# Kernel optimization log

Hardware: AMD Instinct MI355X
Metric: run time of the kernel (lower is better)

## Reference

```python
import jax, jax.numpy as jnp
import numpy as np

NB_KNN = (10, 20, 100, 200)   # values of k to evaluate; max_k = 200
T = 0.07                       # softmax temperature
NUM_CLASSES = 1000


def setup_inputs() -> dict:
    key = jax.random.key(0)
    k1, k2, k3 = jax.random.split(key, 3)
    features_rank = jax.random.normal(k1, (256, 512), jnp.float32)      # (B, d) query features
    train_features = jax.random.normal(k2, (100000, 512), jnp.float32)  # (N, d) train bank
    train_labels = jax.random.randint(k3, (100000,), 0, NUM_CLASSES)     # (N,) int labels
    return {"features_rank": features_rank, "train_features": train_features,
            "train_labels": train_labels}


def _knn_probs(features_rank, train_features, train_labels):
    max_k = max(NB_KNN)
    # similarity: (B, N) = (B, d) @ (d, N)  -- mirrors torch.mm(broadcasted, train_features_rank_T)
    sims = features_rank @ train_features.T
    topk_sims, idx = jax.lax.top_k(sims, max_k)          # (B, max_k), sorted descending
    neighbors = train_labels[idx]                         # (B, max_k) gathered labels
    w = jax.nn.softmax(topk_sims / T, axis=1)             # (B, max_k) neighbor weights
    B = features_rank.shape[0]
    rows = jnp.arange(B)[:, None]                         # (B, 1) row indices for scatter
    # Instead of materializing one_hot (B, max_k, C) and summing prefixes,
    # scatter-add the first k weights into per-class buckets (same math, fused).
    probs = [jnp.zeros((B, NUM_CLASSES), w.dtype).at[rows, neighbors[:, :k]].add(w[:, :k])
             for k in NB_KNN]
    return jnp.stack(probs, axis=0)                       # (len(NB_KNN), B, C)


def reference(features_rank, train_features, train_labels):
    return _knn_probs(features_rank, train_features, train_labels)
```

## Files before the change

kernel.cpp:

```cpp
#include <hip/hip_runtime.h>
#include <math.h>

#define KDIM   512
#define NCLS   1000
#define CUTOFF 3.0f
#define MAXCAP 4096
#define BN     64
#define BK     64
#define NSTAGE (KDIM / BK)
#define FCAP   512

typedef __attribute__((ext_vector_type(8))) short  short8;
typedef __attribute__((ext_vector_type(4))) float  floatx4;

__device__ __forceinline__ unsigned enc_f(float f) {
    unsigned u = __float_as_uint(f);
    return (u & 0x80000000u) ? ~u : (u | 0x80000000u);
}
__device__ __forceinline__ float dec_f(unsigned k) {
    unsigned u = (k & 0x80000000u) ? (k & 0x7FFFFFFFu) : ~k;
    return __uint_as_float(u);
}
__device__ __forceinline__ unsigned short f2bf(float f) {
    unsigned u = __float_as_uint(f);
    u += 0x7FFFu + ((u >> 16) & 1u);
    return (unsigned short)(u >> 16);
}
__device__ __forceinline__ float bf2f(unsigned short h) {
    return __uint_as_float(((unsigned)h) << 16);
}

__global__ void k_prep(const float* __restrict__ A, unsigned short* __restrict__ af,
                       unsigned* __restrict__ cnt, unsigned* __restrict__ gmax, int Brows) {
    int t = blockIdx.x * blockDim.x + threadIdx.x;
    if (t < Brows) { cnt[t] = 0u; gmax[t] = enc_f(-3.0e38f); }
    if (t >= Brows * (KDIM / 8)) return;
    int r = t >> 6;
    int o = t & 63;
    int s16 = r >> 4, c = o >> 2, kq = o & 3;
    int lane = kq * 16 + (r & 15);
    const float* src = A + (size_t)r * KDIM + o * 8;
    size_t bhi = ((size_t)((s16 * 16 + c) * 2 + 0) * 64 + lane) * 8;
    size_t blo = ((size_t)((s16 * 16 + c) * 2 + 1) * 64 + lane) * 8;
#pragma unroll
    for (int j = 0; j < 8; ++j) {
        float f = src[j];
        unsigned short h = f2bf(f);
        af[bhi + j] = h;
        af[blo + j] = f2bf(f - bf2f(h));
    }
}

__global__ __launch_bounds__(256, 3) void k_gemm(
    const float* __restrict__ Bt,
    const unsigned short* __restrict__ af,
    float* __restrict__ cand_val, int* __restrict__ cand_idx,
    unsigned* __restrict__ cnt, unsigned* __restrict__ gmax,
    int N, int cap)
{
    __shared__ short8 BsH[2][512];
    __shared__ short8 BsL[2][512];

    const int tid  = threadIdx.x;
    const int lane = tid & 63;
    const int wid  = tid >> 6;
    const int colBase = blockIdx.x * BN;

    const int nl   = tid >> 2;
    const int kseg = (tid & 3) * 16;
    const int gcol = colBase + nl;
    const bool colok = (gcol < N);
    const float* bsrc = Bt + (size_t)gcol * KDIM + kseg;

    int slotw[2];
#pragma unroll
    for (int oo = 0; oo < 2; ++oo) {
        const int k8  = kseg + oo * 8;
        const int chw = k8 >> 5;
        const int kqw = (k8 >> 3) & 3;
        const int ctw = (nl >> 4) & 3;
        const int fidw = chw * 4 + ctw;
        const int lfw  = kqw * 16 + (nl & 15);
        slotw[oo] = fidw * 64 + (lfw ^ (kqw * 2 + chw));
    }

    floatx4 acc[4][4];
#pragma unroll
    for (int rt = 0; rt < 4; ++rt)
#pragma unroll
        for (int ct = 0; ct < 4; ++ct)
            acc[rt][ct] = (floatx4){0.f, 0.f, 0.f, 0.f};

    const float4 z4 = make_float4(0.f, 0.f, 0.f, 0.f);
    float4 c0 = colok ? *(const float4*)(bsrc)           : z4;
    float4 c1 = colok ? *(const float4*)(bsrc + 4)       : z4;
    float4 c2 = colok ? *(const float4*)(bsrc + 8)       : z4;
    float4 c3 = colok ? *(const float4*)(bsrc + 12)      : z4;
    float4 n0 = colok ? *(const float4*)(bsrc + BK)      : z4;
    float4 n1 = colok ? *(const float4*)(bsrc + BK + 4)  : z4;
    float4 n2 = colok ? *(const float4*)(bsrc + BK + 8)  : z4;
    float4 n3 = colok ? *(const float4*)(bsrc + BK + 12) : z4;

    auto cvw = [&](int buf, float4 a0, float4 a1, float4 a2, float4 a3) {
        union { float4 v[4]; float f[16]; } P;
        P.v[0] = a0; P.v[1] = a1; P.v[2] = a2; P.v[3] = a3;
#pragma unroll
        for (int oo = 0; oo < 2; ++oo) {
            union { short8 v; unsigned short u[8]; } H, L;
#pragma unroll
            for (int j = 0; j < 8; ++j) {
                float f = P.f[oo * 8 + j];
                unsigned short h = f2bf(f);
                H.u[j] = h; L.u[j] = f2bf(f - bf2f(h));
            }
            BsH[buf][slotw[oo]] = H.v;
            BsL[buf][slotw[oo]] = L.v;
        }
    };

    cvw(0, c0, c1, c2, c3);
    __syncthreads();

    for (int s = 0; s < NSTAGE; ++s) {
        if (s + 1 < NSTAGE) {
            c0 = n0; c1 = n1; c2 = n2; c3 = n3;
            if (s + 2 < NSTAGE) {
                const float* p = bsrc + (s + 2) * BK;
                n0 = colok ? *(const float4*)(p)      : z4;
                n1 = colok ? *(const float4*)(p + 4)  : z4;
                n2 = colok ? *(const float4*)(p + 8)  : z4;
                n3 = colok ? *(const float4*)(p + 12) : z4;
            }
            cvw((s + 1) & 1, c0, c1, c2, c3);
        }

#pragma unroll
        for (int chunk = 0; chunk < 2; ++chunk) {
            const int cg = s * 2 + chunk;
            short8 aH[4], aL[4];
#pragma unroll
            for (int rt = 0; rt < 4; ++rt) {
                const int s16 = wid * 4 + rt;
                size_t sl = (size_t)((s16 * 16 + cg) * 2) * 64 + lane;
                aH[rt] = *(const short8*)(af + sl * 8);
                aL[rt] = *(const short8*)(af + (sl + 64) * 8);
            }
            const int g = (lane >> 4) * 2 + chunk;
#pragma unroll
            for (int ct = 0; ct < 4; ++ct) {
                const int idx = (chunk * 4 + ct) * 64 + (lane ^ g);
                short8 bh = BsH[s & 1][idx];
                short8 bl = BsL[s & 1][idx];
#pragma unroll
                for (int rt = 0; rt < 4; ++rt) {
                    acc[rt][ct] = __builtin_amdgcn_mfma_f32_16x16x32_bf16(aH[rt], bh, acc[rt][ct], 0, 0, 0);
                    acc[rt][ct] = __builtin_amdgcn_mfma_f32_16x16x32_bf16(aH[rt], bl, acc[rt][ct], 0, 0, 0);
                    acc[rt][ct] = __builtin_amdgcn_mfma_f32_16x16x32_bf16(aL[rt], bh, acc[rt][ct], 0, 0, 0);
                }
            }
        }
        __syncthreads();
    }

    const int q   = lane >> 4;
    const int n15 = lane & 15;
#pragma unroll
    for (int rt = 0; rt < 4; ++rt) {
#pragma unroll
        for (int reg = 0; reg < 4; ++reg) {
            const int row = wid * 64 + rt * 16 + q * 4 + reg;
            float m = fmaxf(fmaxf(acc[rt][0][reg], acc[rt][1][reg]),
                            fmaxf(acc[rt][2][reg], acc[rt][3][reg]));
#pragma unroll
            for (int off = 1; off < 16; off <<= 1) m = fmaxf(m, __shfl_xor(m, off));
            unsigned oldk = 0u;
            if (n15 == 0) oldk = atomicMax(&gmax[row], enc_f(m));
            oldk = (unsigned)__shfl((int)oldk, lane & 48);
            const float thr = fmaxf(dec_f(oldk), m) - CUTOFF;
#pragma unroll
            for (int ct = 0; ct < 4; ++ct) {
                const float v = acc[rt][ct][reg];
                const int col = colBase + ct * 16 + n15;
                if (v >= thr && col < N) {
                    unsigned p = atomicAdd(&cnt[row], 1u);
                    if (p < (unsigned)cap) {
                        cand_val[(size_t)row * cap + p] = v;
                        cand_idx[(size_t)row * cap + p] = col;
                    }
                }
            }
        }
    }
}

__global__ __launch_bounds__(256) void k_finalize(
    const float* __restrict__ cand_val,
    const int* __restrict__ cand_idx,
    const unsigned* __restrict__ cnt,
    const unsigned* __restrict__ gmax,
    const int* __restrict__ labels,
    float* __restrict__ out,
    int Brows, int cap)
{
    __shared__ float s_val[FCAP];
    __shared__ int   s_idx[FCAP];
    __shared__ float s_out[4 * NCLS];
    __shared__ int   s_n;
    __shared__ float s_part[4];
    __shared__ float s_Z;

    const int row = blockIdx.x;
    const int tid = threadIdx.x;
    if (tid == 0) s_n = 0;
    __syncthreads();

    const float m   = dec_f(gmax[row]);
    const float thr = m - CUTOFF;
    const int n = min((int)cnt[row], cap);
    for (int i = tid; i < n; i += 256) {
        float v = cand_val[(size_t)row * cap + i];
        if (v >= thr) {
            int p = atomicAdd(&s_n, 1);
            if (p < FCAP) { s_val[p] = v; s_idx[p] = cand_idx[(size_t)row * cap + i]; }
        }
    }
    for (int c = tid; c < 4 * NCLS; c += 256) s_out[c] = 0.f;
    __syncthreads();
    const int ns = min(s_n, FCAP);

    float e0 = 0.f, e1 = 0.f;
    int   r0 = 0x7fffffff, r1 = 0x7fffffff;
    int   lab0 = 0, lab1 = 0;
    if (tid < ns) {
        const float v = s_val[tid]; const int ix = s_idx[tid];
        int rk = 0;
        for (int j = 0; j < ns; ++j) {
            const float vj = s_val[j];
            rk += (vj > v || (vj == v && s_idx[j] < ix)) ? 1 : 0;
        }
        r0 = rk;
        if (rk < 200) { e0 = expf((v - m) * (1.0f / 0.07f)); lab0 = labels[ix]; }
    }
    if (tid + 256 < ns) {
        const int i2 = tid + 256;
        const float v = s_val[i2]; const int ix = s_idx[i2];
        int rk = 0;
        for (int j = 0; j < ns; ++j) {
            const float vj = s_val[j];
            rk += (vj > v || (vj == v && s_idx[j] < ix)) ? 1 : 0;
        }
        r1 = rk;
        if (rk < 200) { e1 = expf((v - m) * (1.0f / 0.07f)); lab1 = labels[ix]; }
    }

    float part = e0 + e1;
#pragma unroll
    for (int off = 32; off >= 1; off >>= 1) part += __shfl_down(part, off);
    if ((tid & 63) == 0) s_part[tid >> 6] = part;
    __syncthreads();
    if (tid == 0) s_Z = (s_part[0] + s_part[1]) + (s_part[2] + s_part[3]);
    __syncthreads();
    const float invZ = 1.0f / s_Z;

    if (r0 < 200) {
        const float w = e0 * invZ;
        if (r0 < 10)  atomicAdd(&s_out[0 * NCLS + lab0], w);
        if (r0 < 20)  atomicAdd(&s_out[1 * NCLS + lab0], w);
        if (r0 < 100) atomicAdd(&s_out[2 * NCLS + lab0], w);
        atomicAdd(&s_out[3 * NCLS + lab0], w);
    }
    if (r1 < 200) {
        const float w = e1 * invZ;
        if (r1 < 10)  atomicAdd(&s_out[0 * NCLS + lab1], w);
        if (r1 < 20)  atomicAdd(&s_out[1 * NCLS + lab1], w);
        if (r1 < 100) atomicAdd(&s_out[2 * NCLS + lab1], w);
        atomicAdd(&s_out[3 * NCLS + lab1], w);
    }
    __syncthreads();

    for (int c = tid; c < 4 * NCLS; c += 256) {
        const int sl = c / NCLS, cc = c - sl * NCLS;
        out[(size_t)sl * ((size_t)Brows * NCLS) + (size_t)row * NCLS + cc] = s_out[c];
    }
}

extern "C" void kernel_launch(void* const* d_in, const int* in_sizes, int n_in,
                              void* d_out, int out_size, void* d_ws, size_t ws_size,
                              hipStream_t stream) {
    const float* A      = (const float*)d_in[0];
    const float* Bt     = (const float*)d_in[1];
    const int*   labels = (const int*)d_in[2];
    float* out = (float*)d_out;

    const int Brows = in_sizes[0] / KDIM;
    const int N     = in_sizes[2];

    size_t af_elems = (size_t)Brows * KDIM * 2;
    unsigned short* af = (unsigned short*)d_ws;
    unsigned* cnt  = (unsigned*)(af + af_elems);
    unsigned* gmax = cnt + Brows;
    char* rest = (char*)(gmax + Brows);
    size_t used  = (size_t)(rest - (char*)d_ws);
    size_t avail = (ws_size > used) ? (ws_size - used) : 0;
    int cap = (int)((avail / ((size_t)Brows * 8)) < (size_t)MAXCAP
                        ? (avail / ((size_t)Brows * 8)) : (size_t)MAXCAP);
    if (cap < 1) cap = 1;
    float* cand_val = (float*)rest;
    int*   cand_idx = (int*)(cand_val + (size_t)Brows * cap);

    k_prep<<<(Brows * (KDIM / 8) + 255) / 256, 256, 0, stream>>>(A, af, cnt, gmax, Brows);
    k_gemm<<<(N + BN - 1) / BN, 256, 0, stream>>>(Bt, af, cand_val, cand_idx, cnt, gmax, N, cap);
    k_finalize<<<Brows, 256, 0, stream>>>(cand_val, cand_idx, cnt, gmax, labels, out, Brows, cap);
}
```

Measured before the change: 412.2 us.

## Widen GEMM column tile to 128 with 8 waves each covering 32 rows

The similarity GEMM block now handles 128 train columns with 512 threads (8 waves) instead of 64 columns with 256 threads. Each wave covers 32 query rows by 128 columns (2x8 MFMA tiles) rather than 64x64. This halves the number of blocks, so each block re-reads the bf16-split A operand from global memory for twice as many columns, and the per-wave A fragment loads are cut in half. The cost is double the LDS per block and a different register mix, which may change occupancy, and each wave now reads more B fragments from LDS.

Result: faster. 385.5 us (-6.5%).

```diff
diff --git a/kernel.cpp b/kernel.cpp
--- a/kernel.cpp
+++ b/kernel.cpp
@@ -5,7 +5,7 @@
 #define NCLS   1000
 #define CUTOFF 3.0f
 #define MAXCAP 4096
-#define BN     64
+#define BN     128
 #define BK     64
 #define NSTAGE (KDIM / BK)
 #define FCAP   512
@@ -51,108 +51,103 @@
     }
 }
 
-__global__ __launch_bounds__(256, 3) void k_gemm(
+__global__ __launch_bounds__(512, 3) void k_gemm(
     const float* __restrict__ Bt,
     const unsigned short* __restrict__ af,
     float* __restrict__ cand_val, int* __restrict__ cand_idx,
     unsigned* __restrict__ cnt, unsigned* __restrict__ gmax,
     int N, int cap)
 {
-    __shared__ short8 BsH[2][512];
-    __shared__ short8 BsL[2][512];
+    __shared__ short8 BsH[2][1024];
+    __shared__ short8 BsL[2][1024];
 
     const int tid  = threadIdx.x;
     const int lane = tid & 63;
     const int wid  = tid >> 6;
     const int colBase = blockIdx.x * BN;
 
-    const int nl   = tid >> 2;
-    const int kseg = (tid & 3) * 16;
-    const int gcol = colBase + nl;
-    const bool colok = (gcol < N);
-    const float* bsrc = Bt + (size_t)gcol * KDIM + kseg;
-
-    int slotw[2];
-#pragma unroll
-    for (int oo = 0; oo < 2; ++oo) {
-        const int k8  = kseg + oo * 8;
-        const int chw = k8 >> 5;
-        const int kqw = (k8 >> 3) & 3;
-        const int ctw = (nl >> 4) & 3;
-        const int fidw = chw * 4 + ctw;
-        const int lfw  = kqw * 16 + (nl & 15);
-        slotw[oo] = fidw * 64 + (lfw ^ (kqw * 2 + chw));
-    }
-
-    floatx4 acc[4][4];
-#pragma unroll
-    for (int rt = 0; rt < 4; ++rt)
-#pragma unroll
-        for (int ct = 0; ct < 4; ++ct)
+    const int nl  = tid >> 3;
+    const int k8  = (tid & 7) * 8;
+    const int gcol0 = colBase + nl;
+    const int gcol1 = colBase + 64 + nl;
+    const bool ok0 = (gcol0 < N);
+    const bool ok1 = (gcol1 < N);
+    const float* bsrc0 = Bt + (size_t)gcol0 * KDIM + k8;
+    const float* bsrc1 = Bt + (size_t)gcol1 * KDIM + k8;
+    const int chw = k8 >> 5;
+    const int kqw = (k8 >> 3) & 3;
+    const int ctw = (nl >> 4) & 3;
+    const int fidw = chw * 4 + ctw;
+    const int lfw  = kqw * 16 + (nl & 15);
+    const int slotw = fidw * 64 + (lfw ^ (kqw * 2 + chw));
+
+    floatx4 acc[2][8];
+#pragma unroll
+    for (int rt = 0; rt < 2; ++rt)
+#pragma unroll
+        for (int ct = 0; ct < 8; ++ct)
             acc[rt][ct] = (floatx4){0.f, 0.f, 0.f, 0.f};
 
     const float4 z4 = make_float4(0.f, 0.f, 0.f, 0.f);
-    float4 c0 = colok ? *(const float4*)(bsrc)           : z4;
-    float4 c1 = colok ? *(const float4*)(bsrc + 4)       : z4;
-    float4 c2 = colok ? *(const float4*)(bsrc + 8)       : z4;
-    float4 c3 = colok ? *(const float4*)(bsrc + 12)      : z4;
-    float4 n0 = colok ? *(const float4*)(bsrc + BK)      : z4;
-    float4 n1 = colok ? *(const float4*)(bsrc + BK + 4)  : z4;
-    float4 n2 = colok ? *(const float4*)(bsrc + BK + 8)  : z4;
-    float4 n3 = colok ? *(const float4*)(bsrc + BK + 12) : z4;
-
-    auto cvw = [&](int buf, float4 a0, float4 a1, float4 a2, float4 a3) {
-        union { float4 v[4]; float f[16]; } P;
-        P.v[0] = a0; P.v[1] = a1; P.v[2] = a2; P.v[3] = a3;
-#pragma unroll
-        for (int oo = 0; oo < 2; ++oo) {
-            union { short8 v; unsigned short u[8]; } H, L;
-#pragma unroll
-            for (int j = 0; j < 8; ++j) {
-                float f = P.f[oo * 8 + j];
-                unsigned short h = f2bf(f);
-                H.u[j] = h; L.u[j] = f2bf(f - bf2f(h));
-            }
-            BsH[buf][slotw[oo]] = H.v;
-            BsL[buf][slotw[oo]] = L.v;
-        }
+    float4 c00 = ok0 ? *(const float4*)(bsrc0)          : z4;
+    float4 c01 = ok0 ? *(const float4*)(bsrc0 + 4)      : z4;
+    float4 c10 = ok1 ? *(const float4*)(bsrc1)          : z4;
+    float4 c11 = ok1 ? *(const float4*)(bsrc1 + 4)      : z4;
+    float4 n00 = ok0 ? *(const float4*)(bsrc0 + BK)     : z4;
+    float4 n01 = ok0 ? *(const float4*)(bsrc0 + BK + 4) : z4;
+    float4 n10 = ok1 ? *(const float4*)(bsrc1 + BK)     : z4;
+    float4 n11 = ok1 ? *(const float4*)(bsrc1 + BK + 4) : z4;
+
+    auto cvw = [&](int buf, int off, float4 a0, float4 a1) {
+        union { float4 v[2]; float f[8]; } P;
+        union { short8 v; unsigned short u[8]; } H, L;
+        P.v[0] = a0; P.v[1] = a1;
+#pragma unroll
+        for (int j = 0; j < 8; ++j) {
+            unsigned short h = f2bf(P.f[j]);
+            H.u[j] = h; L.u[j] = f2bf(P.f[j] - bf2f(h));
+        }
+        BsH[buf][off + slotw] = H.v; BsL[buf][off + slotw] = L.v;
     };
 
-    cvw(0, c0, c1, c2, c3);
+    cvw(0, 0,   c00, c01);
+    cvw(0, 512, c10, c11);
     __syncthreads();
 
     for (int s = 0; s < NSTAGE; ++s) {
         if (s + 1 < NSTAGE) {
-            c0 = n0; c1 = n1; c2 = n2; c3 = n3;
+            c00 = n00; c01 = n01; c10 = n10; c11 = n11;
             if (s + 2 < NSTAGE) {
-                const float* p = bsrc + (s + 2) * BK;
-                n0 = colok ? *(const float4*)(p)      : z4;
-                n1 = colok ? *(const float4*)(p + 4)  : z4;
-                n2 = colok ? *(const float4*)(p + 8)  : z4;
-                n3 = colok ? *(const float4*)(p + 12) : z4;
+                const float* p0 = bsrc0 + (s + 2) * BK;
+                const float* p1 = bsrc1 + (s + 2) * BK;
+                n00 = ok0 ? *(const float4*)(p0)     : z4;
+                n01 = ok0 ? *(const float4*)(p0 + 4) : z4;
+                n10 = ok1 ? *(const float4*)(p1)     : z4;
+                n11 = ok1 ? *(const float4*)(p1 + 4) : z4;
             }
-            cvw((s + 1) & 1, c0, c1, c2, c3);
+            cvw((s + 1) & 1, 0,   c00, c01);
+            cvw((s + 1) & 1, 512, c10, c11);
         }
 
 #pragma unroll
         for (int chunk = 0; chunk < 2; ++chunk) {
             const int cg = s * 2 + chunk;
-            short8 aH[4], aL[4];
-#pragma unroll
-            for (int rt = 0; rt < 4; ++rt) {
-                const int s16 = wid * 4 + rt;
+            short8 aH[2], aL[2];
+#pragma unroll
+            for (int rt = 0; rt < 2; ++rt) {
+                const int s16 = wid * 2 + rt;
                 size_t sl = (size_t)((s16 * 16 + cg) * 2) * 64 + lane;
                 aH[rt] = *(const short8*)(af + sl * 8);
                 aL[rt] = *(const short8*)(af + (sl + 64) * 8);
             }
             const int g = (lane >> 4) * 2 + chunk;
 #pragma unroll
-            for (int ct = 0; ct < 4; ++ct) {
-                const int idx = (chunk * 4 + ct) * 64 + (lane ^ g);
+            for (int ct = 0; ct < 8; ++ct) {
+                const int idx = (chunk * 4 + (ct & 3)) * 64 + (lane ^ g) + ((ct & 4) ? 512 : 0);
                 short8 bh = BsH[s & 1][idx];
                 short8 bl = BsL[s & 1][idx];
 #pragma unroll
-                for (int rt = 0; rt < 4; ++rt) {
+                for (int rt = 0; rt < 2; ++rt) {
                     acc[rt][ct] = __builtin_amdgcn_mfma_f32_16x16x32_bf16(aH[rt], bh, acc[rt][ct], 0, 0, 0);
                     acc[rt][ct] = __builtin_amdgcn_mfma_f32_16x16x32_bf16(aH[rt], bl, acc[rt][ct], 0, 0, 0);
                     acc[rt][ct] = __builtin_amdgcn_mfma_f32_16x16x32_bf16(aL[rt], bh, acc[rt][ct], 0, 0, 0);
@@ -165,12 +160,13 @@
     const int q   = lane >> 4;
     const int n15 = lane & 15;
 #pragma unroll
-    for (int rt = 0; rt < 4; ++rt) {
+    for (int rt = 0; rt < 2; ++rt) {
 #pragma unroll
         for (int reg = 0; reg < 4; ++reg) {
-            const int row = wid * 64 + rt * 16 + q * 4 + reg;
-            float m = fmaxf(fmaxf(acc[rt][0][reg], acc[rt][1][reg]),
-                            fmaxf(acc[rt][2][reg], acc[rt][3][reg]));
+            const int row = wid * 32 + rt * 16 + q * 4 + reg;
+            float m = acc[rt][0][reg];
+#pragma unroll
+            for (int ct = 1; ct < 8; ++ct) m = fmaxf(m, acc[rt][ct][reg]);
 #pragma unroll
             for (int off = 1; off < 16; off <<= 1) m = fmaxf(m, __shfl_xor(m, off));
             unsigned oldk = 0u;
@@ -178,9 +174,9 @@
             oldk = (unsigned)__shfl((int)oldk, lane & 48);
             const float thr = fmaxf(dec_f(oldk), m) - CUTOFF;
 #pragma unroll
-            for (int ct = 0; ct < 4; ++ct) {
+            for (int ct = 0; ct < 8; ++ct) {
                 const float v = acc[rt][ct][reg];
-                const int col = colBase + ct * 16 + n15;
+                const int col = colBase + ((ct & 4) ? 64 : 0) + (ct & 3) * 16 + n15;
                 if (v >= thr && col < N) {
                     unsigned p = atomicAdd(&cnt[row], 1u);
                     if (p < (unsigned)cap) {
@@ -309,6 +305,6 @@
     int*   cand_idx = (int*)(cand_val + (size_t)Brows * cap);
 
     k_prep<<<(Brows * (KDIM / 8) + 255) / 256, 256, 0, stream>>>(A, af, cnt, gmax, Brows);
-    k_gemm<<<(N + BN - 1) / BN, 256, 0, stream>>>(Bt, af, cand_val, cand_idx, cnt, gmax, N, cap);
+    k_gemm<<<(N + BN - 1) / BN, 512, 0, stream>>>(Bt, af, cand_val, cand_idx, cnt, gmax, N, cap);
     k_finalize<<<Brows, 256, 0, stream>>>(cand_val, cand_idx, cnt, gmax, labels, out, Brows, cap);
 }
```

## Use 512-thread GEMM blocks with halved per-wave row tiles and hoisted A loads

Applied to the files above, without the earlier changes.

Doubles the GEMM block to 8 waves, so each wave covers 32 query rows instead of 64 and each thread converts 8 B elements per stage instead of 16. The A fragments for both chunks are now loaded before the B conversion and the block barrier, and MFMA issue priority is raised during the inner loop. The aim is lower register pressure and more waves in flight to hide global and LDS latency. Each block still covers the same columns, so there are more waves contending for the same LDS tile and one extra barrier per stage.

Result: faster. 386.2 us (-6.3%).

```diff
diff --git a/kernel.cpp b/kernel.cpp
--- a/kernel.cpp
+++ b/kernel.cpp
@@ -51,7 +51,7 @@
     }
 }
 
-__global__ __launch_bounds__(256, 3) void k_gemm(
+__global__ __launch_bounds__(512, 4) void k_gemm(
     const float* __restrict__ Bt,
     const unsigned short* __restrict__ af,
     float* __restrict__ cand_val, int* __restrict__ cand_idx,
@@ -66,85 +66,81 @@
     const int wid  = tid >> 6;
     const int colBase = blockIdx.x * BN;
 
-    const int nl   = tid >> 2;
-    const int kseg = (tid & 3) * 16;
+    const int nl  = tid >> 3;
+    const int k8  = (tid & 7) * 8;
     const int gcol = colBase + nl;
     const bool colok = (gcol < N);
-    const float* bsrc = Bt + (size_t)gcol * KDIM + kseg;
-
-    int slotw[2];
-#pragma unroll
-    for (int oo = 0; oo < 2; ++oo) {
-        const int k8  = kseg + oo * 8;
-        const int chw = k8 >> 5;
-        const int kqw = (k8 >> 3) & 3;
-        const int ctw = (nl >> 4) & 3;
-        const int fidw = chw * 4 + ctw;
-        const int lfw  = kqw * 16 + (nl & 15);
-        slotw[oo] = fidw * 64 + (lfw ^ (kqw * 2 + chw));
-    }
-
-    floatx4 acc[4][4];
-#pragma unroll
-    for (int rt = 0; rt < 4; ++rt)
+    const float* bsrc = Bt + (size_t)gcol * KDIM + k8;
+    const int chw = k8 >> 5;
+    const int kqw = (k8 >> 3) & 3;
+    const int ctw = (nl >> 4) & 3;
+    const int fidw = chw * 4 + ctw;
+    const int lfw  = kqw * 16 + (nl & 15);
+    const int slotw = fidw * 64 + (lfw ^ (kqw * 2 + chw));
+
+    floatx4 acc[2][4];
+#pragma unroll
+    for (int rt = 0; rt < 2; ++rt)
 #pragma unroll
         for (int ct = 0; ct < 4; ++ct)
             acc[rt][ct] = (floatx4){0.f, 0.f, 0.f, 0.f};
 
     const float4 z4 = make_float4(0.f, 0.f, 0.f, 0.f);
-    float4 c0 = colok ? *(const float4*)(bsrc)           : z4;
-    float4 c1 = colok ? *(const float4*)(bsrc + 4)       : z4;
-    float4 c2 = colok ? *(const float4*)(bsrc + 8)       : z4;
-    float4 c3 = colok ? *(const float4*)(bsrc + 12)      : z4;
-    float4 n0 = colok ? *(const float4*)(bsrc + BK)      : z4;
-    float4 n1 = colok ? *(const float4*)(bsrc + BK + 4)  : z4;
-    float4 n2 = colok ? *(const float4*)(bsrc + BK + 8)  : z4;
-    float4 n3 = colok ? *(const float4*)(bsrc + BK + 12) : z4;
-
-    auto cvw = [&](int buf, float4 a0, float4 a1, float4 a2, float4 a3) {
-        union { float4 v[4]; float f[16]; } P;
-        P.v[0] = a0; P.v[1] = a1; P.v[2] = a2; P.v[3] = a3;
-#pragma unroll
-        for (int oo = 0; oo < 2; ++oo) {
-            union { short8 v; unsigned short u[8]; } H, L;
-#pragma unroll
-            for (int j = 0; j < 8; ++j) {
-                float f = P.f[oo * 8 + j];
-                unsigned short h = f2bf(f);
-                H.u[j] = h; L.u[j] = f2bf(f - bf2f(h));
-            }
-            BsH[buf][slotw[oo]] = H.v;
-            BsL[buf][slotw[oo]] = L.v;
-        }
-    };
-
-    cvw(0, c0, c1, c2, c3);
+    float4 c0 = colok ? *(const float4*)(bsrc)          : z4;
+    float4 c1 = colok ? *(const float4*)(bsrc + 4)      : z4;
+    float4 n0 = colok ? *(const float4*)(bsrc + BK)     : z4;
+    float4 n1 = colok ? *(const float4*)(bsrc + BK + 4) : z4;
+
+    {
+        union { float4 v[2]; float f[8]; } P;
+        union { short8 v; unsigned short u[8]; } H, L;
+        P.v[0] = c0; P.v[1] = c1;
+#pragma unroll
+        for (int j = 0; j < 8; ++j) {
+            unsigned short h = f2bf(P.f[j]);
+            H.u[j] = h; L.u[j] = f2bf(P.f[j] - bf2f(h));
+        }
+        BsH[0][slotw] = H.v; BsL[0][slotw] = L.v;
+    }
     __syncthreads();
 
     for (int s = 0; s < NSTAGE; ++s) {
+        short8 aH[2][2], aL[2][2];
+#pragma unroll
+        for (int chunk = 0; chunk < 2; ++chunk) {
+            const int cg = s * 2 + chunk;
+#pragma unroll
+            for (int rt = 0; rt < 2; ++rt) {
+                const int s16 = wid * 2 + rt;
+                size_t sl = (size_t)((s16 * 16 + cg) * 2) * 64 + lane;
+                aH[chunk][rt] = *(const short8*)(af + sl * 8);
+                aL[chunk][rt] = *(const short8*)(af + (sl + 64) * 8);
+            }
+        }
+        __builtin_amdgcn_sched_barrier(0);
+
         if (s + 1 < NSTAGE) {
-            c0 = n0; c1 = n1; c2 = n2; c3 = n3;
+            c0 = n0; c1 = n1;
             if (s + 2 < NSTAGE) {
                 const float* p = bsrc + (s + 2) * BK;
-                n0 = colok ? *(const float4*)(p)      : z4;
-                n1 = colok ? *(const float4*)(p + 4)  : z4;
-                n2 = colok ? *(const float4*)(p + 8)  : z4;
-                n3 = colok ? *(const float4*)(p + 12) : z4;
-            }
-            cvw((s + 1) & 1, c0, c1, c2, c3);
-        }
-
+                n0 = colok ? *(const float4*)(p)     : z4;
+                n1 = colok ? *(const float4*)(p + 4) : z4;
+            }
+            union { float4 v[2]; float f[8]; } P;
+            union { short8 v; unsigned short u[8]; } H, L;
+            P.v[0] = c0; P.v[1] = c1;
+#pragma unroll
+            for (int j = 0; j < 8; ++j) {
+                unsigned short h = f2bf(P.f[j]);
+                H.u[j] = h; L.u[j] = f2bf(P.f[j] - bf2f(h));
+            }
+            BsH[(s + 1) & 1][slotw] = H.v; BsL[(s + 1) & 1][slotw] = L.v;
+        }
+
+        __syncthreads();
+        __builtin_amdgcn_s_setprio(1);
 #pragma unroll
         for (int chunk = 0; chunk < 2; ++chunk) {
-            const int cg = s * 2 + chunk;
-            short8 aH[4], aL[4];
-#pragma unroll
-            for (int rt = 0; rt < 4; ++rt) {
-                const int s16 = wid * 4 + rt;
-                size_t sl = (size_t)((s16 * 16 + cg) * 2) * 64 + lane;
-                aH[rt] = *(const short8*)(af + sl * 8);
-                aL[rt] = *(const short8*)(af + (sl + 64) * 8);
-            }
             const int g = (lane >> 4) * 2 + chunk;
 #pragma unroll
             for (int ct = 0; ct < 4; ++ct) {
@@ -152,23 +148,24 @@
                 short8 bh = BsH[s & 1][idx];
                 short8 bl = BsL[s & 1][idx];
 #pragma unroll
-                for (int rt = 0; rt < 4; ++rt) {
-                    acc[rt][ct] = __builtin_amdgcn_mfma_f32_16x16x32_bf16(aH[rt], bh, acc[rt][ct], 0, 0, 0);
-                    acc[rt][ct] = __builtin_amdgcn_mfma_f32_16x16x32_bf16(aH[rt], bl, acc[rt][ct], 0, 0, 0);
-                    acc[rt][ct] = __builtin_amdgcn_mfma_f32_16x16x32_bf16(aL[rt], bh, acc[rt][ct], 0, 0, 0);
+                for (int rt = 0; rt < 2; ++rt) {
+                    acc[rt][ct] = __builtin_amdgcn_mfma_f32_16x16x32_bf16(aH[chunk][rt], bh, acc[rt][ct], 0, 0, 0);
+                    acc[rt][ct] = __builtin_amdgcn_mfma_f32_16x16x32_bf16(aH[chunk][rt], bl, acc[rt][ct], 0, 0, 0);
+                    acc[rt][ct] = __builtin_amdgcn_mfma_f32_16x16x32_bf16(aL[chunk][rt], bh, acc[rt][ct], 0, 0, 0);
                 }
             }
         }
+        __builtin_amdgcn_s_setprio(0);
         __syncthreads();
     }
 
     const int q   = lane >> 4;
     const int n15 = lane & 15;
 #pragma unroll
-    for (int rt = 0; rt < 4; ++rt) {
+    for (int rt = 0; rt < 2; ++rt) {
 #pragma unroll
         for (int reg = 0; reg < 4; ++reg) {
-            const int row = wid * 64 + rt * 16 + q * 4 + reg;
+            const int row = wid * 32 + rt * 16 + q * 4 + reg;
             float m = fmaxf(fmaxf(acc[rt][0][reg], acc[rt][1][reg]),
                             fmaxf(acc[rt][2][reg], acc[rt][3][reg]));
 #pragma unroll
@@ -309,6 +306,6 @@
     int*   cand_idx = (int*)(cand_val + (size_t)Brows * cap);
 
     k_prep<<<(Brows * (KDIM / 8) + 255) / 256, 256, 0, stream>>>(A, af, cnt, gmax, Brows);
-    k_gemm<<<(N + BN - 1) / BN, 256, 0, stream>>>(Bt, af, cand_val, cand_idx, cnt, gmax, N, cap);
+    k_gemm<<<(N + BN - 1) / BN, 512, 0, stream>>>(Bt, af, cand_val, cand_idx, cnt, gmax, N, cap);
     k_finalize<<<Brows, 256, 0, stream>>>(cand_val, cand_idx, cnt, gmax, labels, out, Brows, cap);
 }
```
